# Performance work log

Hardware: AMD Instinct MI355X
Metric: run time of the kernel (lower is better)

Reference implementation:

```python
import jax, jax.numpy as jnp
import numpy as np

N_STATE, N_OBS, BATCH, T_LEN = 256, 128, 64, 1024
RICCATI_ITERS = 300


def _steady_state_gain(A, H, Q, R, iters=RICCATI_ITERS):
    """Riccati iteration for the steady-state Kalman gain (numpy, fp64)."""
    n = A.shape[0]
    I = np.eye(n)
    P = np.eye(n)
    for _ in range(iters):
        Pp = A @ P @ A.T + Q
        S = H @ Pp @ H.T + R
        K = np.linalg.solve(S, (Pp @ H.T).T).T
        P = (I - K @ H) @ Pp
    return K


def setup_inputs() -> dict:
    rng = np.random.default_rng(0)
    # Stable dynamics: scaled orthogonal matrix (spectral radius 0.95).
    M = rng.standard_normal((N_STATE, N_STATE))
    Qm, _ = np.linalg.qr(M)
    A = 0.95 * Qm
    H = rng.standard_normal((N_OBS, N_STATE)) / np.sqrt(N_STATE)
    Qc = 0.1 * np.eye(N_STATE)
    Rc = 0.1 * np.eye(N_OBS)
    K = _steady_state_gain(A, H, Qc, Rc)

    key = jax.random.key(0)
    y = jax.random.normal(key, (BATCH, T_LEN, N_OBS), dtype=jnp.float32)
    return {
        "y": y,
        "A": jnp.asarray(A, dtype=jnp.float32),
        "H": jnp.asarray(H, dtype=jnp.float32),
        "K": jnp.asarray(K, dtype=jnp.float32),
    }


def reference(y, A, H, K):
    """Steady-state Kalman filter: x_t = (I - K H) A x_{t-1} + K y_t.

    y: [B, T, n_obs] -> out: [B, T, n_state]
    """
    n = A.shape[0]
    I = jnp.eye(n, dtype=A.dtype)
    A_eff = (I - K @ H) @ A  # [n, n]

    x0 = y[:, 0] @ K.T  # [B, n]

    def step(x, yt):
        x = x @ A_eff.T + yt @ K.T  # [B, n]
        return x, x

    ys = jnp.swapaxes(y[:, 1:], 0, 1)  # [T-1, B, n_obs]
    _, xs = jax.lax.scan(step, x0, ys)  # xs: [T-1, B, n]
    out = jnp.concatenate([x0[:, None, :], jnp.swapaxes(xs, 0, 1)], axis=1)
    return out  # [B, T, n_state]
```

## Files before the change

### kernel.cpp

```cpp
#include <hip/hip_runtime.h>
#include <hip/hip_bf16.h>

#define NS 256
#define MO 128
#define BB 64
#define TT 1024

typedef short s16x8 __attribute__((ext_vector_type(8)));
typedef float f32x4 __attribute__((ext_vector_type(4)));
typedef unsigned int uint;
typedef unsigned short ushort;

__device__ __forceinline__ ushort f2bf(float x) {
    uint u = __float_as_uint(x);
    uint r = (u + 0x7fffu + ((u >> 16) & 1u)) >> 16;
    return (ushort)r;
}
__device__ __forceinline__ float bf2f(ushort h) { return __uint_as_float(((uint)h) << 16); }

__device__ __forceinline__ uint pkbf2(float a, float b) {
    __hip_bfloat162 h = __float22bfloat162_rn(make_float2(a, b));
    union { __hip_bfloat162 b2; uint u; } cv;
    cv.b2 = h;
    return cv.u;
}

__device__ __forceinline__ void conv8(float4 f0, float4 f1, s16x8& vh, s16x8& vl) {
    uint h0 = pkbf2(f0.x, f0.y), h1 = pkbf2(f0.z, f0.w);
    uint h2 = pkbf2(f1.x, f1.y), h3 = pkbf2(f1.z, f1.w);
    float r0 = f0.x - __uint_as_float(h0 << 16);
    float r1 = f0.y - __uint_as_float(h0 & 0xffff0000u);
    float r2 = f0.z - __uint_as_float(h1 << 16);
    float r3 = f0.w - __uint_as_float(h1 & 0xffff0000u);
    float r4 = f1.x - __uint_as_float(h2 << 16);
    float r5 = f1.y - __uint_as_float(h2 & 0xffff0000u);
    float r6 = f1.z - __uint_as_float(h3 << 16);
    float r7 = f1.w - __uint_as_float(h3 & 0xffff0000u);
    uint l0 = pkbf2(r0, r1), l1 = pkbf2(r2, r3);
    uint l2 = pkbf2(r4, r5), l3 = pkbf2(r6, r7);
    union { uint u[4]; s16x8 v; } ch, cl;
    ch.u[0] = h0; ch.u[1] = h1; ch.u[2] = h2; ch.u[3] = h3;
    cl.u[0] = l0; cl.u[1] = l1; cl.u[2] = l2; cl.u[3] = l3;
    vh = ch.v; vl = cl.v;
}

__device__ __forceinline__ f32x4 mfma16(s16x8 a, s16x8 b, f32x4 c) {
    return __builtin_amdgcn_mfma_f32_16x16x32_bf16(a, b, c, 0, 0, 0);
}


__global__ void khaeff_kernel(const float* __restrict__ K, const float* __restrict__ H,
                              const float* __restrict__ A, float* __restrict__ AE,
                              ushort* __restrict__ kah,
                              ushort* __restrict__ aeh, ushort* __restrict__ ael) {
    int i = blockIdx.x, j = threadIdx.x;
    __shared__ float kl[MO];
    __shared__ float khr[NS];
    if (j < MO) {
        float v = K[i * MO + j];
        kl[j] = v;
        kah[i * MO + j] = f2bf(v);
    }
    __syncthreads();
    float acc = 0.f;
#pragma unroll 8
    for (int k = 0; k < MO; ++k) acc += kl[k] * H[k * NS + j];
    khr[j] = acc;
    __syncthreads();
    float ae = A[i * NS + j];
#pragma unroll 8
    for (int k = 0; k < NS; ++k) ae -= khr[k] * A[k * NS + j];
    AE[i * NS + j] = ae;
    ushort hi = f2bf(ae);
    aeh[i * NS + j] = hi;
    ael[i * NS + j] = f2bf(ae - bf2f(hi));
}

__global__ void matsq_kernel(const float* __restrict__ src, float* __restrict__ dst,
                             ushort* dh, ushort* dl) {
    int i = blockIdx.x, j = threadIdx.x;
    __shared__ float row[NS];
    row[j] = src[i * NS + j];
    __syncthreads();
    float acc = 0.f;
#pragma unroll 8
    for (int k = 0; k < NS; ++k) acc += row[k] * src[k * NS + j];
    dst[i * NS + j] = acc;
    if (dh) {
        ushort hi = f2bf(acc);
        dh[i * NS + j] = hi;
        dl[i * NS + j] = f2bf(acc - bf2f(hi));
    }
}


template <int MODE>
__launch_bounds__(512, 1)
__global__ void scan16_kernel(const ushort* __restrict__ mh, const ushort* __restrict__ ml,
                              const ushort* __restrict__ kah,
                              const float* __restrict__ y_g, const ushort* __restrict__ ub,
                              const ushort* __restrict__ cin, float* outf,
                              ushort* __restrict__ wbf, ushort* __restrict__ ebf) {
    constexpr bool YF = (MODE == 0 || MODE == 4);
    constexpr int S = YF ? 16 : ((MODE == 1) ? 8 : 7);
    const int tid = threadIdx.x, blk = blockIdx.x;
    const int w = tid >> 6, l = tid & 63, lr = l & 15, lg = l >> 4;

    __shared__ ushort xh_s[2][16 * NS];
    __shared__ ushort xl_s[2][16 * NS];

    s16x8 Bh[2][8], Bl[2][8];
#pragma unroll
    for (int t2 = 0; t2 < 2; ++t2) {
        int row = 16 * (2 * w + t2) + lr;
#pragma unroll
        for (int q = 0; q < 8; ++q) {
            int off = row * NS + 32 * q + 8 * lg;
            Bh[t2][q] = *(const s16x8*)(mh + off);
            Bl[t2][q] = *(const s16x8*)(ml + off);
        }
    }

    s16x8 KAh[2][4];
    if constexpr (YF) {
#pragma unroll
        for (int t2 = 0; t2 < 2; ++t2) {
            int row = 16 * (2 * w + t2) + lr;
#pragma unroll
            for (int q = 0; q < 4; ++q) {
                KAh[t2][q] = *(const s16x8*)(kah + row * MO + 32 * q + 8 * lg);
            }
        }
    }

    const int b0 = (blk & 3) * 16;
    const int cc = blk >> 2;

#pragma unroll
    for (int jj = 0; jj < 8; ++jj) {
        int idx = jj * 512 + tid;
        int m = idx >> 8, col = idx & 255;
        ushort hu = 0;
        if constexpr (MODE == 3) {
            int rid = blk * 16 + m;
            int b = rid >> 3, g = rid & 7;
            hu = cin[((long)b * 8 + g) * NS + col];
            wbf[((long)b * 64 + 8 * g) * NS + col] = hu;
        } else if constexpr (MODE == 4) {
            hu = cin[((long)(b0 + m) * 64 + cc) * NS + col];
        } else if constexpr (MODE == 2) {
            wbf[(long)(blk * 16 + m) * 8 * NS + col] = 0;
        }
        int si = (m * NS + col) ^ ((m & 7) << 3);
        xh_s[0][si] = hu;
        xl_s[0][si] = 0;
    }

    const int st0 = 32 * w + 4 * lg;
    const int st1 = st0 + 16;

    long ybase = 0, ubase = 0;
    if constexpr (YF) {
        ybase = ((long)(b0 + lr) * TT + cc * 16) * MO + 8 * lg;
    } else if constexpr (MODE == 1 || MODE == 3) {
        int rid = blk * 16 + lr;
        ubase = ((long)(rid >> 3) * 64 + 8 * (rid & 7)) * NS;
    } else {
        ubase = (long)(blk * 16 + lr) * 8 * NS;
    }

    auto ldu = [&](long off) -> f32x4 {
        uint2 v = *(const uint2*)(ub + off);
        return f32x4{__uint_as_float(v.x << 16), __uint_as_float(v.x & 0xffff0000u),
                     __uint_as_float(v.y << 16), __uint_as_float(v.y & 0xffff0000u)};
    };

    float4 yraw[8];
    auto load_y = [&](int s) {
#pragma unroll
        for (int q = 0; q < 4; ++q) {
            long off = ybase + (long)s * MO + 32 * q;
            yraw[2 * q] = *(const float4*)(y_g + off);
            yraw[2 * q + 1] = *(const float4*)(y_g + off + 4);
        }
    };

    auto compute_u = [&](f32x4& ua0, f32x4& ua1) {
        ua0 = f32x4{0.f, 0.f, 0.f, 0.f};
        ua1 = f32x4{0.f, 0.f, 0.f, 0.f};
#pragma unroll
        for (int q = 0; q < 4; ++q) {
            s16x8 yh, yl;
            conv8(yraw[2 * q], yraw[2 * q + 1], yh, yl);
            ua0 = mfma16(KAh[0][q], yh, ua0);
            ua0 = mfma16(KAh[0][q], yl, ua0);
            ua1 = mfma16(KAh[1][q], yh, ua1);
            ua1 = mfma16(KAh[1][q], yl, ua1);
        }
    };

    f32x4 up0, up1;
    if constexpr (YF) {
        load_y(0);
        compute_u(up0, up1);
    } else {
        up0 = ldu(ubase + st0);
        up1 = ldu(ubase + st1);
    }
    __syncthreads();

    for (int s = 0; s < S; ++s) {
        const int cur = s & 1, nxt = cur ^ 1;

        if constexpr (YF) {
            if (s + 1 < S) load_y(s + 1);
        }

        f32x4 a0a = up0, a0b = {0.f, 0.f, 0.f, 0.f}, a0c = {0.f, 0.f, 0.f, 0.f};
        f32x4 a1a = up1, a1b = {0.f, 0.f, 0.f, 0.f}, a1c = {0.f, 0.f, 0.f, 0.f};
#pragma unroll
        for (int q = 0; q < 8; ++q) {
            int ridx = (lr * NS + 32 * q + 8 * lg) ^ ((lr & 7) << 3);
            s16x8 xh = *(const s16x8*)&xh_s[cur][ridx];
            s16x8 xl = *(const s16x8*)&xl_s[cur][ridx];
            a0a = mfma16(Bh[0][q], xh, a0a);
            a0b = mfma16(Bh[0][q], xl, a0b);
            a0c = mfma16(Bl[0][q], xh, a0c);
            a1a = mfma16(Bh[1][q], xh, a1a);
            a1b = mfma16(Bh[1][q], xl, a1b);
            a1c = mfma16(Bl[1][q], xh, a1c);
        }
        f32x4 acc0 = (a0a + a0b) + a0c;
        f32x4 acc1 = (a1a + a1b) + a1c;

        if (s + 1 < S) {
            if constexpr (YF) {
                compute_u(up0, up1);
            } else {
                up0 = ldu(ubase + (long)(s + 1) * NS + st0);
                up1 = ldu(ubase + (long)(s + 1) * NS + st1);
            }
        }

        uint h01a = pkbf2(acc0[0], acc0[1]), h23a = pkbf2(acc0[2], acc0[3]);
        uint h01b = pkbf2(acc1[0], acc1[1]), h23b = pkbf2(acc1[2], acc1[3]);

        if constexpr (MODE == 2) {
            long wb = ((long)(blk * 16 + lr) * 8 + s + 1) * NS;
            *(uint2*)(wbf + wb + st0) = make_uint2(h01a, h23a);
            *(uint2*)(wbf + wb + st1) = make_uint2(h01b, h23b);
        } else if constexpr (MODE == 3) {
            int rid = blk * 16 + lr;
            long wb = ((long)(rid >> 3) * 64 + 8 * (rid & 7) + s + 1) * NS;
            *(uint2*)(wbf + wb + st0) = make_uint2(h01a, h23a);
            *(uint2*)(wbf + wb + st1) = make_uint2(h01b, h23b);
        } else if constexpr (MODE == 4) {
            long ob = ((long)(b0 + lr) * TT + cc * 16 + s) * NS;
            *(f32x4*)(outf + ob + st0) = acc0;
            *(f32x4*)(outf + ob + st1) = acc1;
        } else if constexpr (MODE == 0) {
            if (s == S - 1) {
                long eb = ((long)(b0 + lr) * 64 + cc) * NS;
                *(uint2*)(ebf + eb + st0) = make_uint2(h01a, h23a);
                *(uint2*)(ebf + eb + st1) = make_uint2(h01b, h23b);
            }
        } else if constexpr (MODE == 1) {
            if (s == S - 1) {
                int rid = blk * 16 + lr;
                long eb = ((long)(rid >> 3) * 8 + (rid & 7)) * NS;
                *(uint2*)(ebf + eb + st0) = make_uint2(h01a, h23a);
                *(uint2*)(ebf + eb + st1) = make_uint2(h01b, h23b);
            }
        }

        if (s + 1 < S) {
            float la0 = acc0[0] - __uint_as_float(h01a << 16);
            float la1 = acc0[1] - __uint_as_float(h01a & 0xffff0000u);
            float la2 = acc0[2] - __uint_as_float(h23a << 16);
            float la3 = acc0[3] - __uint_as_float(h23a & 0xffff0000u);
            float lb0 = acc1[0] - __uint_as_float(h01b << 16);
            float lb1 = acc1[1] - __uint_as_float(h01b & 0xffff0000u);
            float lb2 = acc1[2] - __uint_as_float(h23b << 16);
            float lb3 = acc1[3] - __uint_as_float(h23b & 0xffff0000u);
            int wi0 = lr * NS + (st0 ^ ((lr & 7) << 3));
            int wi1 = lr * NS + (st1 ^ ((lr & 7) << 3));
            *(uint2*)&xh_s[nxt][wi0] = make_uint2(h01a, h23a);
            *(uint2*)&xh_s[nxt][wi1] = make_uint2(h01b, h23b);
            *(uint2*)&xl_s[nxt][wi0] = make_uint2(pkbf2(la0, la1), pkbf2(la2, la3));
            *(uint2*)&xl_s[nxt][wi1] = make_uint2(pkbf2(lb0, lb1), pkbf2(lb2, lb3));
        }
        __syncthreads();
    }
}


extern "C" void kernel_launch(void* const* d_in, const int* in_sizes, int n_in,
                              void* d_out, int out_size, void* d_ws, size_t ws_size,
                              hipStream_t stream) {
    const float* y = (const float*)d_in[0];
    const float* A = (const float*)d_in[1];
    const float* H = (const float*)d_in[2];
    const float* K = (const float*)d_in[3];
    float* out = (float*)d_out;

    float* ws = (float*)d_ws;
    const long MAT = (long)NS * NS;
    float* AE = ws + 0 * MAT;
    float* Ta = ws + 1 * MAT;
    float* Tb = ws + 2 * MAT;
    ushort* us = (ushort*)(ws + 3 * MAT);
    ushort* aeh = us;
    ushort* ael = aeh + MAT;
    ushort* mh = ael + MAT;
    ushort* ml = mh + MAT;
    ushort* m2h = ml + MAT;
    ushort* m2l = m2h + MAT;
    ushort* kah = m2l + MAT;
    ushort* e_buf = kah + (long)NS * MO;
    ushort* cbuf = e_buf + (long)BB * 64 * NS;
    ushort* e2 = cbuf + (long)BB * 64 * NS;
    ushort* c2 = e2 + (long)BB * 8 * NS;

    khaeff_kernel<<<NS, NS, 0, stream>>>(K, H, A, AE, kah, aeh, ael);
    matsq_kernel<<<NS, NS, 0, stream>>>(AE, Ta, nullptr, nullptr);
    matsq_kernel<<<NS, NS, 0, stream>>>(Ta, Tb, nullptr, nullptr);
    matsq_kernel<<<NS, NS, 0, stream>>>(Tb, Ta, nullptr, nullptr);
    matsq_kernel<<<NS, NS, 0, stream>>>(Ta, Tb, mh, ml);
    matsq_kernel<<<NS, NS, 0, stream>>>(Tb, Ta, nullptr, nullptr);
    matsq_kernel<<<NS, NS, 0, stream>>>(Ta, Tb, nullptr, nullptr);
    matsq_kernel<<<NS, NS, 0, stream>>>(Tb, Ta, m2h, m2l);

    scan16_kernel<0><<<256, 512, 0, stream>>>(aeh, ael, kah, y, nullptr, nullptr, nullptr, nullptr, e_buf);
    scan16_kernel<1><<<32, 512, 0, stream>>>(mh, ml, nullptr, nullptr, e_buf, nullptr, nullptr, nullptr, e2);
    scan16_kernel<2><<<4, 512, 0, stream>>>(m2h, m2l, nullptr, nullptr, e2, nullptr, nullptr, c2, nullptr);
    scan16_kernel<3><<<32, 512, 0, stream>>>(mh, ml, nullptr, nullptr, e_buf, c2, nullptr, cbuf, nullptr);
    scan16_kernel<4><<<256, 512, 0, stream>>>(aeh, ael, kah, y, nullptr, cbuf, out, nullptr, nullptr);
}
```

Before: 256.0 us.

## Fuse setup and middle scan stages into persistent kernels with grid barriers

Replaces the eight separate setup launches (A_eff build plus seven matrix squarings) with one 256-block kernel that uses atomic grid barriers between squaring passes. The three middle scan stages (modes 1-3) become one 32-block kernel with grid barriers, so the pipeline drops from thirteen launches to four plus a memset. The goal is to remove kernel launch gaps and drain and fill time on a latency-bound chain of small kernels. The spin barriers depend on every block being co-resident; 256 blocks should fit on MI355X's CU count, but nothing in the code guarantees co-residency, and the added memset and atomic polling have their own cost.

```diff
diff --git a/kernel.cpp b/kernel.cpp
--- a/kernel.cpp
+++ b/kernel.cpp
@@ -48,14 +48,29 @@
     return __builtin_amdgcn_mfma_f32_16x16x32_bf16(a, b, c, 0, 0, 0);
 }
 
-
-__global__ void khaeff_kernel(const float* __restrict__ K, const float* __restrict__ H,
-                              const float* __restrict__ A, float* __restrict__ AE,
-                              ushort* __restrict__ kah,
-                              ushort* __restrict__ aeh, ushort* __restrict__ ael) {
-    int i = blockIdx.x, j = threadIdx.x;
+__device__ __forceinline__ void grid_barrier(int* ctr, int target) {
+    __syncthreads();
+    if (threadIdx.x == 0) {
+        __threadfence();
+        atomicAdd(ctr, 1);
+        while (atomicAdd(ctr, 0) < target) { }
+        __threadfence();
+    }
+    __syncthreads();
+}
+
+__global__ void setup_kernel(const float* __restrict__ K, const float* __restrict__ H,
+                             const float* __restrict__ A,
+                             float* __restrict__ Ta, float* __restrict__ Tb,
+                             ushort* __restrict__ kah,
+                             ushort* __restrict__ aeh, ushort* __restrict__ ael,
+                             ushort* __restrict__ mh, ushort* __restrict__ ml,
+                             ushort* __restrict__ m2h, ushort* __restrict__ m2l,
+                             int* bars) {
+    const int i = blockIdx.x, j = threadIdx.x;
     __shared__ float kl[MO];
-    __shared__ float khr[NS];
+    __shared__ float rowb[NS];
+
     if (j < MO) {
         float v = K[i * MO + j];
         kl[j] = v;
@@ -65,49 +80,53 @@
     float acc = 0.f;
 #pragma unroll 8
     for (int k = 0; k < MO; ++k) acc += kl[k] * H[k * NS + j];
-    khr[j] = acc;
+    rowb[j] = acc;
     __syncthreads();
     float ae = A[i * NS + j];
 #pragma unroll 8
-    for (int k = 0; k < NS; ++k) ae -= khr[k] * A[k * NS + j];
-    AE[i * NS + j] = ae;
+    for (int k = 0; k < NS; ++k) ae -= rowb[k] * A[k * NS + j];
+    Ta[i * NS + j] = ae;
     ushort hi = f2bf(ae);
     aeh[i * NS + j] = hi;
     ael[i * NS + j] = f2bf(ae - bf2f(hi));
-}
-
-__global__ void matsq_kernel(const float* __restrict__ src, float* __restrict__ dst,
-                             ushort* dh, ushort* dl) {
-    int i = blockIdx.x, j = threadIdx.x;
-    __shared__ float row[NS];
-    row[j] = src[i * NS + j];
-    __syncthreads();
-    float acc = 0.f;
+    grid_barrier(&bars[0], 256);
+
+    const float* src = Ta;
+    float* dst = Tb;
+#pragma unroll 1
+    for (int p = 1; p <= 7; ++p) {
+        rowb[j] = src[i * NS + j];
+        __syncthreads();
+        float a2 = 0.f;
 #pragma unroll 8
-    for (int k = 0; k < NS; ++k) acc += row[k] * src[k * NS + j];
-    dst[i * NS + j] = acc;
-    if (dh) {
-        ushort hi = f2bf(acc);
-        dh[i * NS + j] = hi;
-        dl[i * NS + j] = f2bf(acc - bf2f(hi));
-    }
-}
-
+        for (int k = 0; k < NS; ++k) a2 += rowb[k] * src[k * NS + j];
+        dst[i * NS + j] = a2;
+        if (p == 4) {
+            ushort h2 = f2bf(a2);
+            mh[i * NS + j] = h2;
+            ml[i * NS + j] = f2bf(a2 - bf2f(h2));
+        } else if (p == 7) {
+            ushort h2 = f2bf(a2);
+            m2h[i * NS + j] = h2;
+            m2l[i * NS + j] = f2bf(a2 - bf2f(h2));
+        }
+        grid_barrier(&bars[p], 256);
+        float* t = (float*)src; src = dst; dst = t;
+    }
+}
 
 template <int MODE>
-__launch_bounds__(512, 1)
-__global__ void scan16_kernel(const ushort* __restrict__ mh, const ushort* __restrict__ ml,
-                              const ushort* __restrict__ kah,
-                              const float* __restrict__ y_g, const ushort* __restrict__ ub,
-                              const ushort* __restrict__ cin, float* outf,
-                              ushort* __restrict__ wbf, ushort* __restrict__ ebf) {
-    constexpr bool YF = (MODE == 0 || MODE == 4);
-    constexpr int S = YF ? 16 : ((MODE == 1) ? 8 : 7);
+__device__ __forceinline__ void scan_core(const ushort* __restrict__ mh,
+                                          const ushort* __restrict__ ml,
+                                          const ushort* __restrict__ ub,
+                                          const ushort* __restrict__ cin,
+                                          ushort* __restrict__ wbf,
+                                          ushort* __restrict__ ebf,
+                                          ushort xh_s[2][16 * NS],
+                                          ushort xl_s[2][16 * NS]) {
+    constexpr int S = (MODE == 1) ? 8 : 7;
     const int tid = threadIdx.x, blk = blockIdx.x;
     const int w = tid >> 6, l = tid & 63, lr = l & 15, lg = l >> 4;
-
-    __shared__ ushort xh_s[2][16 * NS];
-    __shared__ ushort xl_s[2][16 * NS];
 
     s16x8 Bh[2][8], Bl[2][8];
 #pragma unroll
@@ -120,21 +139,6 @@
             Bl[t2][q] = *(const s16x8*)(ml + off);
         }
     }
-
-    s16x8 KAh[2][4];
-    if constexpr (YF) {
-#pragma unroll
-        for (int t2 = 0; t2 < 2; ++t2) {
-            int row = 16 * (2 * w + t2) + lr;
-#pragma unroll
-            for (int q = 0; q < 4; ++q) {
-                KAh[t2][q] = *(const s16x8*)(kah + row * MO + 32 * q + 8 * lg);
-            }
-        }
-    }
-
-    const int b0 = (blk & 3) * 16;
-    const int cc = blk >> 2;
 
 #pragma unroll
     for (int jj = 0; jj < 8; ++jj) {
@@ -146,8 +150,6 @@
             int b = rid >> 3, g = rid & 7;
             hu = cin[((long)b * 8 + g) * NS + col];
             wbf[((long)b * 64 + 8 * g) * NS + col] = hu;
-        } else if constexpr (MODE == 4) {
-            hu = cin[((long)(b0 + m) * 64 + cc) * NS + col];
         } else if constexpr (MODE == 2) {
             wbf[(long)(blk * 16 + m) * 8 * NS + col] = 0;
         }
@@ -159,10 +161,8 @@
     const int st0 = 32 * w + 4 * lg;
     const int st1 = st0 + 16;
 
-    long ybase = 0, ubase = 0;
-    if constexpr (YF) {
-        ybase = ((long)(b0 + lr) * TT + cc * 16) * MO + 8 * lg;
-    } else if constexpr (MODE == 1 || MODE == 3) {
+    long ubase;
+    if constexpr (MODE == 1 || MODE == 3) {
         int rid = blk * 16 + lr;
         ubase = ((long)(rid >> 3) * 64 + 8 * (rid & 7)) * NS;
     } else {
@@ -175,46 +175,12 @@
                      __uint_as_float(v.y << 16), __uint_as_float(v.y & 0xffff0000u)};
     };
 
-    float4 yraw[8];
-    auto load_y = [&](int s) {
-#pragma unroll
-        for (int q = 0; q < 4; ++q) {
-            long off = ybase + (long)s * MO + 32 * q;
-            yraw[2 * q] = *(const float4*)(y_g + off);
-            yraw[2 * q + 1] = *(const float4*)(y_g + off + 4);
-        }
-    };
-
-    auto compute_u = [&](f32x4& ua0, f32x4& ua1) {
-        ua0 = f32x4{0.f, 0.f, 0.f, 0.f};
-        ua1 = f32x4{0.f, 0.f, 0.f, 0.f};
-#pragma unroll
-        for (int q = 0; q < 4; ++q) {
-            s16x8 yh, yl;
-            conv8(yraw[2 * q], yraw[2 * q + 1], yh, yl);
-            ua0 = mfma16(KAh[0][q], yh, ua0);
-            ua0 = mfma16(KAh[0][q], yl, ua0);
-            ua1 = mfma16(KAh[1][q], yh, ua1);
-            ua1 = mfma16(KAh[1][q], yl, ua1);
-        }
-    };
-
-    f32x4 up0, up1;
-    if constexpr (YF) {
-        load_y(0);
-        compute_u(up0, up1);
-    } else {
-        up0 = ldu(ubase + st0);
-        up1 = ldu(ubase + st1);
-    }
+    f32x4 up0 = ldu(ubase + st0);
+    f32x4 up1 = ldu(ubase + st1);
     __syncthreads();
 
     for (int s = 0; s < S; ++s) {
         const int cur = s & 1, nxt = cur ^ 1;
-
-        if constexpr (YF) {
-            if (s + 1 < S) load_y(s + 1);
-        }
 
         f32x4 a0a = up0, a0b = {0.f, 0.f, 0.f, 0.f}, a0c = {0.f, 0.f, 0.f, 0.f};
         f32x4 a1a = up1, a1b = {0.f, 0.f, 0.f, 0.f}, a1c = {0.f, 0.f, 0.f, 0.f};
@@ -234,12 +200,8 @@
         f32x4 acc1 = (a1a + a1b) + a1c;
 
         if (s + 1 < S) {
-            if constexpr (YF) {
-                compute_u(up0, up1);
-            } else {
-                up0 = ldu(ubase + (long)(s + 1) * NS + st0);
-                up1 = ldu(ubase + (long)(s + 1) * NS + st1);
-            }
+            up0 = ldu(ubase + (long)(s + 1) * NS + st0);
+            up1 = ldu(ubase + (long)(s + 1) * NS + st1);
         }
 
         uint h01a = pkbf2(acc0[0], acc0[1]), h23a = pkbf2(acc0[2], acc0[3]);
@@ -254,16 +216,6 @@
             long wb = ((long)(rid >> 3) * 64 + 8 * (rid & 7) + s + 1) * NS;
             *(uint2*)(wbf + wb + st0) = make_uint2(h01a, h23a);
             *(uint2*)(wbf + wb + st1) = make_uint2(h01b, h23b);
-        } else if constexpr (MODE == 4) {
-            long ob = ((long)(b0 + lr) * TT + cc * 16 + s) * NS;
-            *(f32x4*)(outf + ob + st0) = acc0;
-            *(f32x4*)(outf + ob + st1) = acc1;
-        } else if constexpr (MODE == 0) {
-            if (s == S - 1) {
-                long eb = ((long)(b0 + lr) * 64 + cc) * NS;
-                *(uint2*)(ebf + eb + st0) = make_uint2(h01a, h23a);
-                *(uint2*)(ebf + eb + st1) = make_uint2(h01b, h23b);
-            }
         } else if constexpr (MODE == 1) {
             if (s == S - 1) {
                 int rid = blk * 16 + lr;
@@ -293,6 +245,167 @@
     }
 }
 
+__launch_bounds__(512, 1)
+__global__ void mid_kernel(const ushort* __restrict__ mh, const ushort* __restrict__ ml,
+                           const ushort* __restrict__ m2h, const ushort* __restrict__ m2l,
+                           const ushort* __restrict__ e_buf, ushort* __restrict__ e2,
+                           ushort* __restrict__ c2, ushort* __restrict__ cbuf,
+                           int* bars) {
+    __shared__ ushort xh_s[2][16 * NS];
+    __shared__ ushort xl_s[2][16 * NS];
+
+    scan_core<1>(mh, ml, e_buf, nullptr, nullptr, e2, xh_s, xl_s);
+    grid_barrier(&bars[8], 32);
+    if (blockIdx.x < 4) {
+        scan_core<2>(m2h, m2l, e2, nullptr, c2, nullptr, xh_s, xl_s);
+    }
+    grid_barrier(&bars[9], 32);
+    scan_core<3>(mh, ml, e_buf, c2, cbuf, nullptr, xh_s, xl_s);
+}
+
+template <int MODE>
+__launch_bounds__(512, 1)
+__global__ void scan16_kernel(const ushort* __restrict__ mh, const ushort* __restrict__ ml,
+                              const ushort* __restrict__ kah,
+                              const float* __restrict__ y_g,
+                              const ushort* __restrict__ cin, float* outf,
+                              ushort* __restrict__ ebf) {
+    constexpr int S = 16;
+    const int tid = threadIdx.x, blk = blockIdx.x;
+    const int w = tid >> 6, l = tid & 63, lr = l & 15, lg = l >> 4;
+
+    __shared__ ushort xh_s[2][16 * NS];
+    __shared__ ushort xl_s[2][16 * NS];
+
+    s16x8 Bh[2][8], Bl[2][8];
+#pragma unroll
+    for (int t2 = 0; t2 < 2; ++t2) {
+        int row = 16 * (2 * w + t2) + lr;
+#pragma unroll
+        for (int q = 0; q < 8; ++q) {
+            int off = row * NS + 32 * q + 8 * lg;
+            Bh[t2][q] = *(const s16x8*)(mh + off);
+            Bl[t2][q] = *(const s16x8*)(ml + off);
+        }
+    }
+    s16x8 KAh[2][4];
+#pragma unroll
+    for (int t2 = 0; t2 < 2; ++t2) {
+        int row = 16 * (2 * w + t2) + lr;
+#pragma unroll
+        for (int q = 0; q < 4; ++q) {
+            KAh[t2][q] = *(const s16x8*)(kah + row * MO + 32 * q + 8 * lg);
+        }
+    }
+
+    const int b0 = (blk & 3) * 16;
+    const int cc = blk >> 2;
+
+#pragma unroll
+    for (int jj = 0; jj < 8; ++jj) {
+        int idx = jj * 512 + tid;
+        int m = idx >> 8, col = idx & 255;
+        ushort hu = 0;
+        if constexpr (MODE == 4) {
+            hu = cin[((long)(b0 + m) * 64 + cc) * NS + col];
+        }
+        int si = (m * NS + col) ^ ((m & 7) << 3);
+        xh_s[0][si] = hu;
+        xl_s[0][si] = 0;
+    }
+
+    const int st0 = 32 * w + 4 * lg;
+    const int st1 = st0 + 16;
+
+    const long ybase = ((long)(b0 + lr) * TT + cc * 16) * MO + 8 * lg;
+
+    float4 yraw[8];
+    auto load_y = [&](int s) {
+#pragma unroll
+        for (int q = 0; q < 4; ++q) {
+            long off = ybase + (long)s * MO + 32 * q;
+            yraw[2 * q] = *(const float4*)(y_g + off);
+            yraw[2 * q + 1] = *(const float4*)(y_g + off + 4);
+        }
+    };
+    auto compute_u = [&](f32x4& ua0, f32x4& ua1) {
+        ua0 = f32x4{0.f, 0.f, 0.f, 0.f};
+        ua1 = f32x4{0.f, 0.f, 0.f, 0.f};
+#pragma unroll
+        for (int q = 0; q < 4; ++q) {
+            s16x8 yh, yl;
+            conv8(yraw[2 * q], yraw[2 * q + 1], yh, yl);
+            ua0 = mfma16(KAh[0][q], yh, ua0);
+            ua0 = mfma16(KAh[0][q], yl, ua0);
+            ua1 = mfma16(KAh[1][q], yh, ua1);
+            ua1 = mfma16(KAh[1][q], yl, ua1);
+        }
+    };
+
+    f32x4 up0, up1;
+    load_y(0);
+    compute_u(up0, up1);
+    __syncthreads();
+
+    for (int s = 0; s < S; ++s) {
+        const int cur = s & 1, nxt = cur ^ 1;
+
+        if (s + 1 < S) load_y(s + 1);
+
+        f32x4 a0a = up0, a0b = {0.f, 0.f, 0.f, 0.f}, a0c = {0.f, 0.f, 0.f, 0.f};
+        f32x4 a1a = up1, a1b = {0.f, 0.f, 0.f, 0.f}, a1c = {0.f, 0.f, 0.f, 0.f};
+#pragma unroll
+        for (int q = 0; q < 8; ++q) {
+            int ridx = (lr * NS + 32 * q + 8 * lg) ^ ((lr & 7) << 3);
+            s16x8 xh = *(const s16x8*)&xh_s[cur][ridx];
+            s16x8 xl = *(const s16x8*)&xl_s[cur][ridx];
+            a0a = mfma16(Bh[0][q], xh, a0a);
+            a0b = mfma16(Bh[0][q], xl, a0b);
+            a0c = mfma16(Bl[0][q], xh, a0c);
+            a1a = mfma16(Bh[1][q], xh, a1a);
+            a1b = mfma16(Bh[1][q], xl, a1b);
+            a1c = mfma16(Bl[1][q], xh, a1c);
+        }
+        f32x4 acc0 = (a0a + a0b) + a0c;
+        f32x4 acc1 = (a1a + a1b) + a1c;
+
+        if (s + 1 < S) compute_u(up0, up1);
+
+        uint h01a = pkbf2(acc0[0], acc0[1]), h23a = pkbf2(acc0[2], acc0[3]);
+        uint h01b = pkbf2(acc1[0], acc1[1]), h23b = pkbf2(acc1[2], acc1[3]);
+
+        if constexpr (MODE == 4) {
+            long ob = ((long)(b0 + lr) * TT + cc * 16 + s) * NS;
+            *(f32x4*)(outf + ob + st0) = acc0;
+            *(f32x4*)(outf + ob + st1) = acc1;
+        } else {
+            if (s == S - 1) {
+                long eb = ((long)(b0 + lr) * 64 + cc) * NS;
+                *(uint2*)(ebf + eb + st0) = make_uint2(h01a, h23a);
+                *(uint2*)(ebf + eb + st1) = make_uint2(h01b, h23b);
+            }
+        }
+
+        if (s + 1 < S) {
+            float la0 = acc0[0] - __uint_as_float(h01a << 16);
+            float la1 = acc0[1] - __uint_as_float(h01a & 0xffff0000u);
+            float la2 = acc0[2] - __uint_as_float(h23a << 16);
+            float la3 = acc0[3] - __uint_as_float(h23a & 0xffff0000u);
+            float lb0 = acc1[0] - __uint_as_float(h01b << 16);
+            float lb1 = acc1[1] - __uint_as_float(h01b & 0xffff0000u);
+            float lb2 = acc1[2] - __uint_as_float(h23b << 16);
+            float lb3 = acc1[3] - __uint_as_float(h23b & 0xffff0000u);
+            int wi0 = lr * NS + (st0 ^ ((lr & 7) << 3));
+            int wi1 = lr * NS + (st1 ^ ((lr & 7) << 3));
+            *(uint2*)&xh_s[nxt][wi0] = make_uint2(h01a, h23a);
+            *(uint2*)&xh_s[nxt][wi1] = make_uint2(h01b, h23b);
+            *(uint2*)&xl_s[nxt][wi0] = make_uint2(pkbf2(la0, la1), pkbf2(la2, la3));
+            *(uint2*)&xl_s[nxt][wi1] = make_uint2(pkbf2(lb0, lb1), pkbf2(lb2, lb3));
+        }
+        __syncthreads();
+    }
+}
+
 
 extern "C" void kernel_launch(void* const* d_in, const int* in_sizes, int n_in,
                               void* d_out, int out_size, void* d_ws, size_t ws_size,
@@ -305,11 +418,10 @@
 
     float* ws = (float*)d_ws;
     const long MAT = (long)NS * NS;
-    float* AE = ws + 0 * MAT;
-    float* Ta = ws + 1 * MAT;
-    float* Tb = ws + 2 * MAT;
-    ushort* us = (ushort*)(ws + 3 * MAT);
-    ushort* aeh = us;
+    float* Ta = ws + 0 * MAT;
+    float* Tb = ws + 1 * MAT;
+    ushort* usb = (ushort*)(ws + 2 * MAT);
+    ushort* aeh = usb;
     ushort* ael = aeh + MAT;
     ushort* mh = ael + MAT;
     ushort* ml = mh + MAT;
@@ -320,19 +432,12 @@
     ushort* cbuf = e_buf + (long)BB * 64 * NS;
     ushort* e2 = cbuf + (long)BB * 64 * NS;
     ushort* c2 = e2 + (long)BB * 8 * NS;
-
-    khaeff_kernel<<<NS, NS, 0, stream>>>(K, H, A, AE, kah, aeh, ael);
-    matsq_kernel<<<NS, NS, 0, stream>>>(AE, Ta, nullptr, nullptr);
-    matsq_kernel<<<NS, NS, 0, stream>>>(Ta, Tb, nullptr, nullptr);
-    matsq_kernel<<<NS, NS, 0, stream>>>(Tb, Ta, nullptr, nullptr);
-    matsq_kernel<<<NS, NS, 0, stream>>>(Ta, Tb, mh, ml);
-    matsq_kernel<<<NS, NS, 0, stream>>>(Tb, Ta, nullptr, nullptr);
-    matsq_kernel<<<NS, NS, 0, stream>>>(Ta, Tb, nullptr, nullptr);
-    matsq_kernel<<<NS, NS, 0, stream>>>(Tb, Ta, m2h, m2l);
-
-    scan16_kernel<0><<<256, 512, 0, stream>>>(aeh, ael, kah, y, nullptr, nullptr, nullptr, nullptr, e_buf);
-    scan16_kernel<1><<<32, 512, 0, stream>>>(mh, ml, nullptr, nullptr, e_buf, nullptr, nullptr, nullptr, e2);
-    scan16_kernel<2><<<4, 512, 0, stream>>>(m2h, m2l, nullptr, nullptr, e2, nullptr, nullptr, c2, nullptr);
-    scan16_kernel<3><<<32, 512, 0, stream>>>(mh, ml, nullptr, nullptr, e_buf, c2, nullptr, cbuf, nullptr);
-    scan16_kernel<4><<<256, 512, 0, stream>>>(aeh, ael, kah, y, nullptr, cbuf, out, nullptr, nullptr);
-}
+    int* bars = (int*)(ws + 26 * MAT);
+
+    hipMemsetAsync(bars, 0, 16 * sizeof(int), stream);
+    setup_kernel<<<256, 256, 0, stream>>>(K, H, A, Ta, Tb, kah, aeh, ael,
+                                          mh, ml, m2h, m2l, bars);
+    scan16_kernel<0><<<256, 512, 0, stream>>>(aeh, ael, kah, y, nullptr, nullptr, e_buf);
+    mid_kernel<<<32, 512, 0, stream>>>(mh, ml, m2h, m2l, e_buf, e2, c2, cbuf, bars);
+    scan16_kernel<4><<<256, 512, 0, stream>>>(aeh, ael, kah, y, cbuf, out, nullptr);
+}
```

Result: slower. 381.8 us (+49.2%).
